# Kernel tuning notes

Measured on AMD Instinct MI355X. Metric: run time of the kernel, lower is better.

## Reference

```python
import jax, jax.numpy as jnp
import numpy as np

H = 51  # num_hidden

def lstm_cell(x, h, c, Wih, Whh, bih, bhh):
    # PyTorch LSTMCell gate order: i, f, g, o
    gates = x @ Wih.T + bih + h @ Whh.T + bhh
    i, f, g, o = jnp.split(gates, 4, axis=-1)
    c_new = jax.nn.sigmoid(f) * c + jax.nn.sigmoid(i) * jnp.tanh(g)
    h_new = jax.nn.sigmoid(o) * jnp.tanh(c_new)
    return h_new, c_new

def setup_inputs() -> dict:
    key = jax.random.key(0)
    ks = jax.random.split(key, 9)
    B, T = 8192, 512
    s1 = 1.0 / np.sqrt(H)  # torch LSTMCell init scale U(-1/sqrt(H), 1/sqrt(H))
    s2 = 1.0
    u = lambda k, shape, s: jax.random.uniform(k, shape, jnp.float32, -s, s)
    return {
        "x": jax.random.normal(ks[0], (B, T), dtype=jnp.float32),
        "Wih1": u(ks[1], (4 * H, 1), s1),
        "Whh1": u(ks[2], (4 * H, H), s1),
        "bih1": u(ks[3], (4 * H,), s1),
        "bhh1": u(ks[4], (4 * H,), s1),
        "Wih2": u(ks[5], (4, H), s2),
        "Whh2": u(ks[6], (4, 1), s2),
        "bih2": u(ks[7], (4,), s2),
        "bhh2": u(ks[8], (4,), s2),
    }

def reference(x, Wih1, Whh1, bih1, bhh1, Wih2, Whh2, bih2, bhh2):
    B, T = x.shape
    xs = x.T[:, :, None]  # [T, B, 1]
    h1 = jnp.zeros((B, H), x.dtype)
    c1 = jnp.zeros((B, H), x.dtype)
    h2 = jnp.zeros((B, 1), x.dtype)
    c2 = jnp.zeros((B, 1), x.dtype)

    def step(carry, xt):
        h1, c1, h2, c2 = carry
        h1, c1 = lstm_cell(xt, h1, c1, Wih1, Whh1, bih1, bhh1)
        h2, c2 = lstm_cell(c1, h2, c2, Wih2, Whh2, bih2, bhh2)
        return (h1, c1, h2, c2), None

    (h1, c1, h2, c2), _ = jax.lax.scan(step, (h1, c1, h2, c2), xs)
    # extra step after the loop (as in the original forward)
    h1, c1 = lstm_cell(c2, h1, c1, Wih1, Whh1, bih1, bhh1)
    h2, output = lstm_cell(c1, h2, c2, Wih2, Whh2, bih2, bhh2)
    return output  # [B, 1] (final cell state of lstm2)
```

## Files before the change

kernel.cpp:

```cpp
#include <hip/hip_runtime.h>

#define TT 512
#define L2E  1.4426950408889634f
#define L2E2 2.8853900817779268f
#define NTHR 320

typedef _Float16 f16;
typedef _Float16 f16x8 __attribute__((ext_vector_type(8)));
typedef float f32x4 __attribute__((ext_vector_type(4)));

__device__ __forceinline__ float fsig_p(float a){
    return __builtin_amdgcn_rcpf(1.f + __builtin_amdgcn_exp2f(-a));
}
__device__ __forceinline__ float ftanhg_p(float a){
    return 2.f * __builtin_amdgcn_rcpf(1.f + __builtin_amdgcn_exp2f(-a)) - 1.f;
}
__device__ __forceinline__ float ftanh_c(float c){
    return 2.f * __builtin_amdgcn_rcpf(1.f + __builtin_amdgcn_exp2f(-L2E2*c)) - 1.f;
}

#define FMA_LO(accv, wd, hh) asm("v_fma_mix_f32 %0, %1, %2, %0 op_sel:[0,0,0] op_sel_hi:[1,0,0]" : "+v"(accv) : "v"(wd), "v"(hh))
#define FMA_HI(accv, wd, hh) asm("v_fma_mix_f32 %0, %1, %2, %0 op_sel:[1,0,0] op_sel_hi:[1,0,0]" : "+v"(accv) : "v"(wd), "v"(hh))

__global__ void repack_w(const float* __restrict__ Whh1, const float* __restrict__ Wih1,
                         const float* __restrict__ bih1, const float* __restrict__ bhh1,
                         const float* __restrict__ Wih2,
                         f16* __restrict__ Wp, f16* __restrict__ Wp2)
{
    int i = blockIdx.x*256 + threadIdx.x;
    if (i < 13*2*64*8) {
        int b    = i & 7;
        int lane = (i >> 3) & 63;
        int kt   = (i >> 9) & 1;
        int m    = i >> 10;
        int r = m*16 + (lane & 15);
        int u = r >> 2, g = r & 3;
        int k = kt*32 + (lane >> 4)*8 + b;
        float v = 0.f;
        if (u < 51) {
            int rt = g*51 + u;
            if      (k < 51)  v = Whh1[rt*51 + k];
            else if (k == 51) v = Wih1[rt];
            else if (k == 52) v = bih1[rt] + bhh1[rt];
            v *= (g == 2) ? L2E2 : L2E;
        }
        Wp[i] = (f16)v;
    }
    if (i < 224) {
        int u = i >> 2, g = i & 3;
        float v = (u < 51) ? Wih2[g*51 + u] : 0.f;
        v *= (g == 2) ? L2E2 : L2E;
        Wp2[i] = (f16)v;
    }
}

__global__ __launch_bounds__(NTHR, 2) void lstm_main(
    const float* __restrict__ X, const f16* __restrict__ Wp, const f16* __restrict__ Wp2,
    const float* __restrict__ Whh2, const float* __restrict__ bih2, const float* __restrict__ bhh2,
    float* __restrict__ out)
{
    __shared__ __align__(16) f16   HB[1024];
    __shared__ __align__(16) float PBL[4][16][4];
    __shared__ __align__(16) f16   HX[TT*16];

    const int tid  = threadIdx.x;
    const int w    = tid >> 6;
    const int lane = tid & 63;
    const int q    = (lane >> 4) & 3;
    const int jl   = lane & 15;
    const int d8   = jl & 7;
    const int bb   = blockIdx.x * 16;

    for (int i = tid; i < 512; i += NTHR) ((unsigned*)HB)[i] = 0u;
    for (int i = tid; i < 256; i += NTHR) ((unsigned*)PBL)[i] = 0u;

    for (int flat = tid*4; flat < 8192; flat += NTHR*4) {
        int row = flat >> 9, col = flat & 511;
        float4 v = *(const float4*)(X + (size_t)(bb + row)*TT + col);
        HX[(col+0)*16 + row] = (f16)v.x;
        HX[(col+1)*16 + row] = (f16)v.y;
        HX[(col+2)*16 + row] = (f16)v.z;
        HX[(col+3)*16 + row] = (f16)v.w;
    }
    __syncthreads();
    if (w == 0 && lane < 16) {
        int dd = lane & 7;
        HB[lane*64 + ((6 ^ dd) << 3) + 4] = (f16)1.f;
        HB[lane*64 + ((6 ^ dd) << 3) + 3] = HX[0*16 + lane];
    }

    const int wv   = (w < 4) ? w : 0;
    const bool has4 = (w == 1);
    const int tiles[4] = { wv, 4+wv, 8+wv, 12 };
    f16x8 A0[4], A1[4];
    uint2 w2p[4];
    #pragma unroll
    for (int k = 0; k < 4; ++k) {
        int m = tiles[k];
        A0[k]  = *(const f16x8*)(Wp + (m*2+0)*512 + lane*8);
        A1[k]  = *(const f16x8*)(Wp + (m*2+1)*512 + lane*8);
        w2p[k] = *(const uint2*)(Wp2 + (m*4+q)*4);
    }
    float wh2[4], bs2[4];
    #pragma unroll
    for (int g = 0; g < 4; ++g) {
        float sc = (g == 2) ? L2E2 : L2E;
        wh2[g] = Whh2[g] * sc;
        bs2[g] = (bih2[g] + bhh2[g]) * sc;
    }

    float c1[4] = {0.f, 0.f, 0.f, 0.f};
    float c2 = 0.f, h2 = 0.f;
    const f32x4 zero4 = {0.f, 0.f, 0.f, 0.f};

    __syncthreads();

    for (int t = 0; t < TT; ++t) {
        f16x8 B0, B1;
        f32x4 S0, S1, S2, S3;
        f16 xn;
        if (w < 4) {
            const f16* rb = HB + jl*64;
            B0 = *(const f16x8*)(rb + ((q       ^ d8) << 3));
            B1 = *(const f16x8*)(rb + (((4 + q) ^ d8) << 3));
        } else {
            S0 = *(const f32x4*)&PBL[0][jl][0];
            S1 = *(const f32x4*)&PBL[1][jl][0];
            S2 = *(const f32x4*)&PBL[2][jl][0];
            S3 = *(const f32x4*)&PBL[3][jl][0];
            xn = HX[((t+1 < TT) ? t+1 : 0)*16 + jl];
        }

        __syncthreads();

        if (w == 4) {
            if (t > 0) {
                f32x4 S = S0 + S1 + S2 + S3;
                float g0 = S[0] + bs2[0] + wh2[0]*h2;
                float g1 = S[1] + bs2[1] + wh2[1]*h2;
                float g2 = S[2] + bs2[2] + wh2[2]*h2;
                float g3 = S[3] + bs2[3] + wh2[3]*h2;
                float i2 = fsig_p(g0), f2 = fsig_p(g1), gg2 = ftanhg_p(g2), o2 = fsig_p(g3);
                c2 = f2*c2 + i2*gg2;
                h2 = o2*ftanh_c(c2);
            }
            if (lane < 16)
                HB[jl*64 + ((6 ^ d8) << 3) + 3] = xn;
        } else {
            float p0 = 0.f, p1 = 0.f, p2 = 0.f, p3 = 0.f;
            #pragma unroll
            for (int k = 0; k < 4; ++k) {
                if (k < 3 || has4) {
                    f32x4 a  = __builtin_amdgcn_mfma_f32_16x16x32_f16(A0[k], B0, zero4, 0,0,0);
                    f32x4 a2 = __builtin_amdgcn_mfma_f32_16x16x32_f16(A1[k], B1, zero4, 0,0,0);
                    a += a2;
                    float ig = fsig_p(a[0]), fg = fsig_p(a[1]), gg = ftanhg_p(a[2]), og = fsig_p(a[3]);
                    float c  = fg*c1[k] + ig*gg;
                    c1[k] = c;
                    int u = tiles[k]*4 + q;
                    if (k < 3 || q < 3)
                        HB[jl*64 + (((u >> 3) ^ d8) << 3) + (u & 7)] = (f16)(og * ftanh_c(c));
                    FMA_LO(p0, w2p[k].x, c); FMA_HI(p1, w2p[k].x, c);
                    FMA_LO(p2, w2p[k].y, c); FMA_HI(p3, w2p[k].y, c);
                }
            }
            p0 += __shfl_xor(p0, 16); p0 += __shfl_xor(p0, 32);
            p1 += __shfl_xor(p1, 16); p1 += __shfl_xor(p1, 32);
            p2 += __shfl_xor(p2, 16); p2 += __shfl_xor(p2, 32);
            p3 += __shfl_xor(p3, 16); p3 += __shfl_xor(p3, 32);
            if (lane < 16) {
                f32x4 pv = {p0, p1, p2, p3};
                *(f32x4*)&PBL[w][jl][0] = pv;
            }
        }
        __syncthreads();
    }

    if (w == 4) {
        f32x4 S = *(const f32x4*)&PBL[0][jl][0];
        S += *(const f32x4*)&PBL[1][jl][0];
        S += *(const f32x4*)&PBL[2][jl][0];
        S += *(const f32x4*)&PBL[3][jl][0];
        float g0 = S[0] + bs2[0] + wh2[0]*h2;
        float g1 = S[1] + bs2[1] + wh2[1]*h2;
        float g2 = S[2] + bs2[2] + wh2[2]*h2;
        float g3 = S[3] + bs2[3] + wh2[3]*h2;
        float i2 = fsig_p(g0), f2 = fsig_p(g1), gg2 = ftanhg_p(g2), o2 = fsig_p(g3);
        c2 = f2*c2 + i2*gg2;
        h2 = o2*ftanh_c(c2);
        if (lane < 16) HB[jl*64 + ((6 ^ d8) << 3) + 3] = (f16)c2;
    }
    __syncthreads();

    if (w < 4) {
        const f16* rb = HB + jl*64;
        f16x8 B0 = *(const f16x8*)(rb + ((q       ^ d8) << 3));
        f16x8 B1 = *(const f16x8*)(rb + (((4 + q) ^ d8) << 3));

        float p0 = 0.f, p1 = 0.f, p2 = 0.f, p3 = 0.f;
        #pragma unroll
        for (int k = 0; k < 4; ++k) {
            if (k < 3 || has4) {
                f32x4 a  = __builtin_amdgcn_mfma_f32_16x16x32_f16(A0[k], B0, zero4, 0,0,0);
                f32x4 a2 = __builtin_amdgcn_mfma_f32_16x16x32_f16(A1[k], B1, zero4, 0,0,0);
                a += a2;
                float ig = fsig_p(a[0]), fg = fsig_p(a[1]), gg = ftanhg_p(a[2]);
                float c  = fg*c1[k] + ig*gg;
                FMA_LO(p0, w2p[k].x, c); FMA_HI(p1, w2p[k].x, c);
                FMA_LO(p2, w2p[k].y, c); FMA_HI(p3, w2p[k].y, c);
            }
        }
        p0 += __shfl_xor(p0, 16); p0 += __shfl_xor(p0, 32);
        p1 += __shfl_xor(p1, 16); p1 += __shfl_xor(p1, 32);
        p2 += __shfl_xor(p2, 16); p2 += __shfl_xor(p2, 32);
        p3 += __shfl_xor(p3, 16); p3 += __shfl_xor(p3, 32);
        if (lane < 16) {
            f32x4 pv = {p0, p1, p2, p3};
            *(f32x4*)&PBL[w][jl][0] = pv;
        }
    }
    __syncthreads();

    if (w == 4) {
        f32x4 S = *(const f32x4*)&PBL[0][jl][0];
        S += *(const f32x4*)&PBL[1][jl][0];
        S += *(const f32x4*)&PBL[2][jl][0];
        S += *(const f32x4*)&PBL[3][jl][0];
        float g0 = S[0] + bs2[0] + wh2[0]*h2;
        float g1 = S[1] + bs2[1] + wh2[1]*h2;
        float g2 = S[2] + bs2[2] + wh2[2]*h2;
        float i2 = fsig_p(g0), f2 = fsig_p(g1), gg2 = ftanhg_p(g2);
        float c2n = f2*c2 + i2*gg2;
        if (lane < 16) out[bb + jl] = c2n;
    }
}

extern "C" void kernel_launch(void* const* d_in, const int* in_sizes, int n_in,
                              void* d_out, int out_size, void* d_ws, size_t ws_size,
                              hipStream_t stream) {
    const float* X    = (const float*)d_in[0];
    const float* Wih1 = (const float*)d_in[1];
    const float* Whh1 = (const float*)d_in[2];
    const float* bih1 = (const float*)d_in[3];
    const float* bhh1 = (const float*)d_in[4];
    const float* Wih2 = (const float*)d_in[5];
    const float* Whh2 = (const float*)d_in[6];
    const float* bih2 = (const float*)d_in[7];
    const float* bhh2 = (const float*)d_in[8];
    float* out = (float*)d_out;

    f16* Wp  = (f16*)d_ws;
    f16* Wp2 = (f16*)((char*)d_ws + 26624);

    repack_w<<<52, 256, 0, stream>>>(Whh1, Wih1, bih1, bhh1, Wih2, Wp, Wp2);
    lstm_main<<<512, NTHR, 0, stream>>>(X, Wp, Wp2, Whh2, bih2, bhh2, out);
}
```

Measured before the change: 489.1 us.

## Spread LSTM gate tiles across seven MFMA waves per block

Raises the block from 5 to 8 waves. Seven compute waves now own at most two gate tiles each instead of four waves owning three or four, and an eighth wave runs the second-layer cell over seven partial sums. The two MFMAs per tile now chain through the accumulator instead of being added separately. The aim is a shorter per-timestep critical path in the serial recurrence. In exchange it adds more waves per barrier, more partial-sum reads for the reducer wave, and possible occupancy pressure, since launch bounds now request 4 blocks of 512 threads.

```diff
diff --git a/kernel.cpp b/kernel.cpp
--- a/kernel.cpp
+++ b/kernel.cpp
@@ -3,7 +3,7 @@
 #define TT 512
 #define L2E  1.4426950408889634f
 #define L2E2 2.8853900817779268f
-#define NTHR 320
+#define NTHR 512
 
 typedef _Float16 f16;
 typedef _Float16 f16x8 __attribute__((ext_vector_type(8)));
@@ -54,13 +54,13 @@
     }
 }
 
-__global__ __launch_bounds__(NTHR, 2) void lstm_main(
+__global__ __launch_bounds__(NTHR, 4) void lstm_main(
     const float* __restrict__ X, const f16* __restrict__ Wp, const f16* __restrict__ Wp2,
     const float* __restrict__ Whh2, const float* __restrict__ bih2, const float* __restrict__ bhh2,
     float* __restrict__ out)
 {
     __shared__ __align__(16) f16   HB[1024];
-    __shared__ __align__(16) float PBL[4][16][4];
+    __shared__ __align__(16) float PBL[7][16][4];
     __shared__ __align__(16) f16   HX[TT*16];
 
     const int tid  = threadIdx.x;
@@ -72,7 +72,7 @@
     const int bb   = blockIdx.x * 16;
 
     for (int i = tid; i < 512; i += NTHR) ((unsigned*)HB)[i] = 0u;
-    for (int i = tid; i < 256; i += NTHR) ((unsigned*)PBL)[i] = 0u;
+    if (tid < 448) ((unsigned*)PBL)[tid] = 0u;
 
     for (int flat = tid*4; flat < 8192; flat += NTHR*4) {
         int row = flat >> 9, col = flat & 511;
@@ -89,13 +89,12 @@
         HB[lane*64 + ((6 ^ dd) << 3) + 3] = HX[0*16 + lane];
     }
 
-    const int wv   = (w < 4) ? w : 0;
-    const bool has4 = (w == 1);
-    const int tiles[4] = { wv, 4+wv, 8+wv, 12 };
-    f16x8 A0[4], A1[4];
-    uint2 w2p[4];
+    const int NT = (w < 6) ? 2 : ((w == 6) ? 1 : 0);
+    const int tiles[2] = { (w < 6) ? 2*w : 12, (w < 6) ? 2*w+1 : 12 };
+    f16x8 A0[2], A1[2];
+    uint2 w2p[2];
     #pragma unroll
-    for (int k = 0; k < 4; ++k) {
+    for (int k = 0; k < 2; ++k) {
         int m = tiles[k];
         A0[k]  = *(const f16x8*)(Wp + (m*2+0)*512 + lane*8);
         A1[k]  = *(const f16x8*)(Wp + (m*2+1)*512 + lane*8);
@@ -109,7 +108,7 @@
         bs2[g] = (bih2[g] + bhh2[g]) * sc;
     }
 
-    float c1[4] = {0.f, 0.f, 0.f, 0.f};
+    float c1[2] = {0.f, 0.f};
     float c2 = 0.f, h2 = 0.f;
     const f32x4 zero4 = {0.f, 0.f, 0.f, 0.f};
 
@@ -117,29 +116,29 @@
 
     for (int t = 0; t < TT; ++t) {
         f16x8 B0, B1;
-        f32x4 S0, S1, S2, S3;
+        f32x4 S[7];
         f16 xn;
-        if (w < 4) {
+        if (w < 7) {
             const f16* rb = HB + jl*64;
             B0 = *(const f16x8*)(rb + ((q       ^ d8) << 3));
             B1 = *(const f16x8*)(rb + (((4 + q) ^ d8) << 3));
         } else {
-            S0 = *(const f32x4*)&PBL[0][jl][0];
-            S1 = *(const f32x4*)&PBL[1][jl][0];
-            S2 = *(const f32x4*)&PBL[2][jl][0];
-            S3 = *(const f32x4*)&PBL[3][jl][0];
+            #pragma unroll
+            for (int k = 0; k < 7; ++k) S[k] = *(const f32x4*)&PBL[k][jl][0];
             xn = HX[((t+1 < TT) ? t+1 : 0)*16 + jl];
         }
 
         __syncthreads();
 
-        if (w == 4) {
+        if (w == 7) {
             if (t > 0) {
-                f32x4 S = S0 + S1 + S2 + S3;
-                float g0 = S[0] + bs2[0] + wh2[0]*h2;
-                float g1 = S[1] + bs2[1] + wh2[1]*h2;
-                float g2 = S[2] + bs2[2] + wh2[2]*h2;
-                float g3 = S[3] + bs2[3] + wh2[3]*h2;
+                f32x4 Ss = S[0];
+                #pragma unroll
+                for (int k = 1; k < 7; ++k) Ss += S[k];
+                float g0 = Ss[0] + bs2[0] + wh2[0]*h2;
+                float g1 = Ss[1] + bs2[1] + wh2[1]*h2;
+                float g2 = Ss[2] + bs2[2] + wh2[2]*h2;
+                float g3 = Ss[3] + bs2[3] + wh2[3]*h2;
                 float i2 = fsig_p(g0), f2 = fsig_p(g1), gg2 = ftanhg_p(g2), o2 = fsig_p(g3);
                 c2 = f2*c2 + i2*gg2;
                 h2 = o2*ftanh_c(c2);
@@ -149,16 +148,15 @@
         } else {
             float p0 = 0.f, p1 = 0.f, p2 = 0.f, p3 = 0.f;
             #pragma unroll
-            for (int k = 0; k < 4; ++k) {
-                if (k < 3 || has4) {
-                    f32x4 a  = __builtin_amdgcn_mfma_f32_16x16x32_f16(A0[k], B0, zero4, 0,0,0);
-                    f32x4 a2 = __builtin_amdgcn_mfma_f32_16x16x32_f16(A1[k], B1, zero4, 0,0,0);
-                    a += a2;
+            for (int k = 0; k < 2; ++k) {
+                if (k < NT) {
+                    f32x4 a = __builtin_amdgcn_mfma_f32_16x16x32_f16(A0[k], B0, zero4, 0,0,0);
+                    a       = __builtin_amdgcn_mfma_f32_16x16x32_f16(A1[k], B1, a,     0,0,0);
                     float ig = fsig_p(a[0]), fg = fsig_p(a[1]), gg = ftanhg_p(a[2]), og = fsig_p(a[3]);
                     float c  = fg*c1[k] + ig*gg;
                     c1[k] = c;
                     int u = tiles[k]*4 + q;
-                    if (k < 3 || q < 3)
+                    if (u < 51)
                         HB[jl*64 + (((u >> 3) ^ d8) << 3) + (u & 7)] = (f16)(og * ftanh_c(c));
                     FMA_LO(p0, w2p[k].x, c); FMA_HI(p1, w2p[k].x, c);
                     FMA_LO(p2, w2p[k].y, c); FMA_HI(p3, w2p[k].y, c);
@@ -176,15 +174,14 @@
         __syncthreads();
     }
 
-    if (w == 4) {
-        f32x4 S = *(const f32x4*)&PBL[0][jl][0];
-        S += *(const f32x4*)&PBL[1][jl][0];
-        S += *(const f32x4*)&PBL[2][jl][0];
-        S += *(const f32x4*)&PBL[3][jl][0];
-        float g0 = S[0] + bs2[0] + wh2[0]*h2;
-        float g1 = S[1] + bs2[1] + wh2[1]*h2;
-        float g2 = S[2] + bs2[2] + wh2[2]*h2;
-        float g3 = S[3] + bs2[3] + wh2[3]*h2;
+    if (w == 7) {
+        f32x4 Ss = *(const f32x4*)&PBL[0][jl][0];
+        #pragma unroll
+        for (int k = 1; k < 7; ++k) Ss += *(const f32x4*)&PBL[k][jl][0];
+        float g0 = Ss[0] + bs2[0] + wh2[0]*h2;
+        float g1 = Ss[1] + bs2[1] + wh2[1]*h2;
+        float g2 = Ss[2] + bs2[2] + wh2[2]*h2;
+        float g3 = Ss[3] + bs2[3] + wh2[3]*h2;
         float i2 = fsig_p(g0), f2 = fsig_p(g1), gg2 = ftanhg_p(g2), o2 = fsig_p(g3);
         c2 = f2*c2 + i2*gg2;
         h2 = o2*ftanh_c(c2);
@@ -192,18 +189,17 @@
     }
     __syncthreads();
 
-    if (w < 4) {
+    if (w < 7) {
         const f16* rb = HB + jl*64;
         f16x8 B0 = *(const f16x8*)(rb + ((q       ^ d8) << 3));
         f16x8 B1 = *(const f16x8*)(rb + (((4 + q) ^ d8) << 3));
 
         float p0 = 0.f, p1 = 0.f, p2 = 0.f, p3 = 0.f;
         #pragma unroll
-        for (int k = 0; k < 4; ++k) {
-            if (k < 3 || has4) {
-                f32x4 a  = __builtin_amdgcn_mfma_f32_16x16x32_f16(A0[k], B0, zero4, 0,0,0);
-                f32x4 a2 = __builtin_amdgcn_mfma_f32_16x16x32_f16(A1[k], B1, zero4, 0,0,0);
-                a += a2;
+        for (int k = 0; k < 2; ++k) {
+            if (k < NT) {
+                f32x4 a = __builtin_amdgcn_mfma_f32_16x16x32_f16(A0[k], B0, zero4, 0,0,0);
+                a       = __builtin_amdgcn_mfma_f32_16x16x32_f16(A1[k], B1, a,     0,0,0);
                 float ig = fsig_p(a[0]), fg = fsig_p(a[1]), gg = ftanhg_p(a[2]);
                 float c  = fg*c1[k] + ig*gg;
                 FMA_LO(p0, w2p[k].x, c); FMA_HI(p1, w2p[k].x, c);
@@ -221,14 +217,13 @@
     }
     __syncthreads();
 
-    if (w == 4) {
-        f32x4 S = *(const f32x4*)&PBL[0][jl][0];
-        S += *(const f32x4*)&PBL[1][jl][0];
-        S += *(const f32x4*)&PBL[2][jl][0];
-        S += *(const f32x4*)&PBL[3][jl][0];
-        float g0 = S[0] + bs2[0] + wh2[0]*h2;
-        float g1 = S[1] + bs2[1] + wh2[1]*h2;
-        float g2 = S[2] + bs2[2] + wh2[2]*h2;
+    if (w == 7) {
+        f32x4 Ss = *(const f32x4*)&PBL[0][jl][0];
+        #pragma unroll
+        for (int k = 1; k < 7; ++k) Ss += *(const f32x4*)&PBL[k][jl][0];
+        float g0 = Ss[0] + bs2[0] + wh2[0]*h2;
+        float g1 = Ss[1] + bs2[1] + wh2[1]*h2;
+        float g2 = Ss[2] + bs2[2] + wh2[2]*h2;
         float i2 = fsig_p(g0), f2 = fsig_p(g1), gg2 = ftanhg_p(g2);
         float c2n = f2*c2 + i2*gg2;
         if (lane < 16) out[bb + jl] = c2n;
```

Measured after the change: 519.8 us. 6.3% more time.
